# Optimization experiments

Hardware: AMD Instinct MI355X
Metric: run time of the kernel (lower is better)

## Reference

```python
import jax, jax.numpy as jnp
import numpy as np

LN_EPS = 1e-5
NORM_EPS = 1e-12  # F.normalize eps


def _l2norm(x):
    # torch F.normalize(p=2, dim=-1): x / max(||x||, eps)
    n = jnp.sqrt(jnp.sum(x * x, axis=-1, keepdims=True))
    return x / jnp.maximum(n, NORM_EPS)


def setup_inputs() -> dict:
    key = jax.random.key(0)
    D, R, H = 256, 32, 64  # d_model, rank, d_model//4
    B, C, P = 32, 64, 96
    ks = jax.random.split(key, 16)
    s = 0.05
    return {
        "x": jax.random.normal(ks[0], (B * C, P, D), jnp.float32),
        "ln_gamma": jnp.ones((D,), jnp.float32),
        "ln_beta": jnp.zeros((D,), jnp.float32),
        "Wd": jax.random.normal(ks[1], (D, R), jnp.float32) * s,
        "bd": jax.random.normal(ks[2], (R,), jnp.float32) * s,
        "Wq": jax.random.normal(ks[3], (R, R), jnp.float32) * s,
        "Wk": jax.random.normal(ks[4], (R, R), jnp.float32) * s,
        "Wv": jax.random.normal(ks[5], (R, R), jnp.float32) * s,
        "Wg": jax.random.normal(ks[6], (R, R), jnp.float32) * s,
        "bg": jax.random.normal(ks[7], (R,), jnp.float32) * s,
        "Wu": jax.random.normal(ks[8], (R, D), jnp.float32) * s,
        "bu": jax.random.normal(ks[9], (D,), jnp.float32) * s,
        "W1": jax.random.normal(ks[10], (D, H), jnp.float32) * s,
        "b1": jax.random.normal(ks[11], (H,), jnp.float32) * s,
        "W2": jax.random.normal(ks[12], (H, D), jnp.float32) * s,
        "b2": jnp.full((D,), -5.0, jnp.float32),  # gate_init bias
        "B": B,
        "C": C,
    }


def reference(x, ln_gamma, ln_beta, Wd, bd, Wq, Wk, Wv, Wg, bg, Wu, bu, W1, b1, W2, b2, B, C):
    BC, P, D = x.shape
    # [B*C, P, D] -> [B*P, C, D] channel-mixing layout
    h = x.reshape(B, C, P, D).transpose(0, 2, 1, 3).reshape(B * P, C, D)

    # LayerNorm over D (biased variance, as in torch LayerNorm)
    mu = jnp.mean(h, axis=-1, keepdims=True)
    var = jnp.var(h, axis=-1, keepdims=True)
    h_norm = (h - mu) * jax.lax.rsqrt(var + LN_EPS) * ln_gamma + ln_beta

    # bottleneck projection to rank R
    h_low = h_norm @ Wd + bd  # [BP, C, R]

    # Hydra linear attention: cosine-normalized Q/K, sum-pooled K*V global feature
    Q = _l2norm(h_low @ Wq)
    K = _l2norm(h_low @ Wk)
    V = h_low @ Wv
    global_feat = jnp.sum(K * V, axis=1, keepdims=True)  # [BP, 1, R]
    h_attn = Q * global_feat

    # content gate and up-projection
    gate_c = jax.nn.sigmoid(h_low @ Wg + bg)
    mixed = (h_attn * gate_c) @ Wu + bu  # [BP, C, D]

    # AdaptiveGate: unbiased variance over channel dim (torch .var default ddof=1)
    chan_var = jnp.var(h, axis=1, ddof=1)  # [BP, D]
    gate_logits = jax.nn.gelu(chan_var @ W1 + b1, approximate=False) @ W2 + b2
    gate = jax.nn.sigmoid(gate_logits)[:, None, :]  # [BP, 1, D]

    out = h + gate * mixed
    # back to [B*C, P, D]
    return out.reshape(B, P, C, D).transpose(0, 2, 1, 3).reshape(BC, P, D)
```

## Files before the change

kernel.cpp:

```cpp
#include <hip/hip_runtime.h>
#include <hip/hip_bf16.h>

#define DD 256
#define RR 32
#define CC 64
#define PB 96
#define NT 1024

typedef __attribute__((ext_vector_type(8))) short short8;
typedef __attribute__((ext_vector_type(4))) float f32x4;

__device__ __forceinline__ short f2bf(float f) {
    return __builtin_bit_cast(short, __float2bfloat16(f));
}
__device__ __forceinline__ float b2f(unsigned short s) {
    union { unsigned u; float f; } v; v.u = ((unsigned)s) << 16;
    return v.f;
}

__device__ __forceinline__ int hswz(int c, int d) {
    return c * 256 + (d ^ ((c & 7) << 3));
}
__device__ __forceinline__ int nswz(int r, int k) {
    return r * 32 + (k ^ (((r >> 1) & 3) << 3));
}

__global__ __launch_bounds__(1024, 1)
void prep_kernel(const float* __restrict__ ln_g, const float* __restrict__ ln_b,
                 const float* __restrict__ Wd, const float* __restrict__ bd,
                 const float* __restrict__ Wq, const float* __restrict__ Wk,
                 const float* __restrict__ Wv, const float* __restrict__ Wg,
                 const float* __restrict__ Wu,
                 const float* __restrict__ W1, const float* __restrict__ W2,
                 short* __restrict__ wsF1, short* __restrict__ wsF2,
                 short* __restrict__ wsF3, float* __restrict__ wsLN,
                 float* __restrict__ wsW1T, float* __restrict__ wsW2T)
{
    __shared__ float redp[2048];
    const int t = threadIdx.x;
    {
        const int r = t >> 5, dblk = t & 31;
        float sa = 0.f, sb = 0.f;
        #pragma unroll
        for (int j = 0; j < 8; ++j) {
            const int d = dblk * 8 + j;
            const float wd = Wd[d * RR + r];
            sa += ln_g[d] * wd;
            sb += ln_b[d] * wd;
        }
        redp[r * 32 + dblk]        = sa;
        redp[1024 + r * 32 + dblk] = sb;
    }
    {
        const int f = t >> 6, l = t & 63;
        const int rt = f >> 3, step = f & 7;
        const int r = rt * 16 + (l & 15);
        short8 v;
        #pragma unroll
        for (int j = 0; j < 8; ++j) {
            const int d = step * 32 + (l >> 4) * 8 + j;
            v[j] = f2bf(ln_g[d] * Wd[d * RR + r]);
        }
        *(short8*)&wsF1[f * 512 + l * 8] = v;
    }
    if (t < 512) {
        const int f = t >> 6, l = t & 63;
        const int m = f >> 1, half = f & 1;
        const float* Wm = (m == 0) ? Wq : (m == 1) ? Wk : (m == 2) ? Wv : Wg;
        const int rout = half * 16 + (l & 15);
        short8 v;
        #pragma unroll
        for (int j = 0; j < 8; ++j) {
            const int rin = (l >> 4) * 8 + j;
            v[j] = f2bf(Wm[rin * RR + rout]);
        }
        *(short8*)&wsF2[f * 512 + l * 8] = v;
    }
    {
        const int f = t >> 6, l = t & 63;
        const int d = f * 16 + (l & 15);
        short8 v;
        #pragma unroll
        for (int j = 0; j < 8; ++j) {
            const int r = (l >> 4) * 8 + j;
            v[j] = f2bf(Wu[r * DD + d]);
        }
        *(short8*)&wsF3[f * 512 + l * 8] = v;
    }
    #pragma unroll
    for (int rep = 0; rep < 16; ++rep) {
        const int id = rep * 1024 + t;
        const int j = id >> 8, d = id & 255;
        wsW1T[j * 256 + d] = W1[d * 64 + j];
    }
    #pragma unroll
    for (int rep = 0; rep < 16; ++rep) {
        const int id = rep * 1024 + t;
        const int d = id >> 6, j = id & 63;
        wsW2T[d * 64 + j] = W2[j * 256 + d];
    }
    __syncthreads();
    if (t < 32) {
        float s = 0.f;
        #pragma unroll
        for (int g = 0; g < 32; ++g) s += redp[t * 32 + g];
        wsLN[t] = s;
    } else if (t < 64) {
        const int r = t - 32;
        float s = 0.f;
        #pragma unroll
        for (int g = 0; g < 32; ++g) s += redp[1024 + r * 32 + g];
        wsLN[t] = s + bd[r];
    }
}

__global__ __launch_bounds__(NT, 8)
void hydra_kernel(const float* __restrict__ x,
                  const short* __restrict__ wsF1, const short* __restrict__ wsF2,
                  const short* __restrict__ wsF3, const float* __restrict__ wsLN,
                  const float* __restrict__ wsW1T, const float* __restrict__ wsW2T,
                  const float* __restrict__ bg,
                  const float* __restrict__ bu,
                  const float* __restrict__ b1, const float* __restrict__ b2,
                  float* __restrict__ out)
{
    __shared__ short hbf[CC * DD];
    __shared__ short qg[CC * RR];
    __shared__ short lowbuf[CC * RR];
    __shared__ float redA[1024];
    __shared__ float redB[2048];
    __shared__ float redC[1024];
    __shared__ float mu_s[CC], rstd_s[CC];
    __shared__ float cv_s[DD], gate_s[DD];
    __shared__ float hid_s[64];
    __shared__ float ln_a[RR], ln_bv[RR];

    const int t    = threadIdx.x;
    const int lane = t & 63;
    const int w    = t >> 6;
    const int bp   = blockIdx.x;
    const int b    = bp / PB;
    const int p    = bp - b * PB;
    const size_t rowbase = (size_t)(b * CC) * PB * DD + (size_t)p * DD;

    #pragma unroll
    for (int i = 0; i < 4; ++i) {
        const int c = w * 4 + i;
        const float4 v = *(const float4*)(x + rowbase + (size_t)c * (PB * DD) + 4 * lane);
        float s1 = v.x + v.y + v.z + v.w;
        float s2 = v.x * v.x + v.y * v.y + v.z * v.z + v.w * v.w;
        s1 += __shfl_xor(s1, 1, 64); s2 += __shfl_xor(s2, 1, 64);
        s1 += __shfl_xor(s1, 2, 64); s2 += __shfl_xor(s2, 2, 64);
        s1 += __shfl_xor(s1, 4, 64); s2 += __shfl_xor(s2, 4, 64);
        if ((lane & 7) == 0)
            *(float2*)&redC[(c * 8 + (lane >> 3)) * 2] = make_float2(s1, s2);
        ushort4 pk;
        pk.x = (unsigned short)f2bf(v.x); pk.y = (unsigned short)f2bf(v.y);
        pk.z = (unsigned short)f2bf(v.z); pk.w = (unsigned short)f2bf(v.w);
        *(ushort4*)&hbf[hswz(c, 4 * lane)] = pk;
    }
    if (t < 32)              ln_a[t]       = wsLN[t];
    else if (t < 64)         ln_bv[t - 32] = wsLN[t];
    __syncthreads();

    f32x4 s3acc = {0.f, 0.f, 0.f, 0.f};
    if (w < 8) {
        const int ct = w >> 1, rt = w & 1;
        const int arow = ct * 16 + (lane & 15);
        const int kofs = (lane >> 4) * 8;
        const short* fB = wsF1 + rt * 8 * 512 + lane * 8;
        #pragma unroll
        for (int step = 0; step < 8; ++step) {
            const short8 bf = *(const short8*)(fB + step * 512);
            const short8 a  = *(const short8*)&hbf[hswz(arow, step * 32 + kofs)];
            s3acc = __builtin_amdgcn_mfma_f32_16x16x32_bf16(a, bf, s3acc, 0, 0, 0);
        }
    } else {
        const int idx = t - 512;
        const int dp  = idx & 127;
        const int rg  = idx >> 7;
        const int d0  = dp * 2;
        float s1a = 0.f, s1b = 0.f, s2a = 0.f, s2b = 0.f;
        #pragma unroll
        for (int i = 0; i < 16; ++i) {
            const int c = rg * 16 + i;
            const ushort2 u = *(const ushort2*)&hbf[hswz(c, d0)];
            const float va = b2f(u.x), vb = b2f(u.y);
            s1a += va; s2a += va * va;
            s1b += vb; s2b += vb * vb;
        }
        *(float2*)&redB[rg * 256 + d0]        = make_float2(s1a, s1b);
        *(float2*)&redB[1024 + rg * 256 + d0] = make_float2(s2a, s2b);
        if (idx < 64) {
            const int c = idx;
            float s1 = 0.f, s2 = 0.f;
            #pragma unroll
            for (int g = 0; g < 8; ++g) {
                const float2 pr = *(const float2*)&redC[(c * 8 + g) * 2];
                s1 += pr.x; s2 += pr.y;
            }
            const float mu = s1 * (1.f / 256.f);
            mu_s[c]   = mu;
            rstd_s[c] = rsqrtf(s2 * (1.f / 256.f) - mu * mu + 1e-5f);
        }
    }
    __syncthreads();

    if (w < 8) {
        const int ct = w >> 1, rt = w & 1;
        const int col = rt * 16 + (lane & 15);
        const float la = ln_a[col], lb = ln_bv[col];
        #pragma unroll
        for (int i = 0; i < 4; ++i) {
            const int c = ct * 16 + (lane >> 4) * 4 + i;
            const float rs = rstd_s[c];
            const float hl = rs * s3acc[i] - rs * mu_s[c] * la + lb;
            lowbuf[nswz(c, col)] = f2bf(hl);
        }
    } else if (t < 768) {
        const int d = t - 512;
        const float S1 = redB[d] + redB[256 + d] + redB[512 + d] + redB[768 + d];
        const float S2 = redB[1024 + d] + redB[1280 + d] + redB[1536 + d] + redB[1792 + d];
        cv_s[d] = (S2 - S1 * S1 * (1.f / 64.f)) * (1.f / 63.f);
    }
    __syncthreads();

    if (w < 8) {
        const int ct = w >> 1, pair = w & 1;
        const int mA = pair ? 1 : 0;
        const int mB = pair ? 2 : 3;
        const int arow = ct * 16 + (lane & 15);
        const int kofs = (lane >> 4) * 8;
        const short8 a = *(const short8*)&lowbuf[nswz(arow, kofs)];
        const short8 bA0 = *(const short8*)(wsF2 + (mA * 2 + 0) * 512 + lane * 8);
        const short8 bA1 = *(const short8*)(wsF2 + (mA * 2 + 1) * 512 + lane * 8);
        const short8 bB0 = *(const short8*)(wsF2 + (mB * 2 + 0) * 512 + lane * 8);
        const short8 bB1 = *(const short8*)(wsF2 + (mB * 2 + 1) * 512 + lane * 8);
        f32x4 aA0 = {0,0,0,0}, aA1 = {0,0,0,0}, aB0 = {0,0,0,0}, aB1 = {0,0,0,0};
        aA0 = __builtin_amdgcn_mfma_f32_16x16x32_bf16(a, bA0, aA0, 0, 0, 0);
        aA1 = __builtin_amdgcn_mfma_f32_16x16x32_bf16(a, bA1, aA1, 0, 0, 0);
        aB0 = __builtin_amdgcn_mfma_f32_16x16x32_bf16(a, bB0, aB0, 0, 0, 0);
        aB1 = __builtin_amdgcn_mfma_f32_16x16x32_bf16(a, bB1, aB1, 0, 0, 0);
        float qs[4];
        #pragma unroll
        for (int i = 0; i < 4; ++i) {
            float ss = aA0[i] * aA0[i] + aA1[i] * aA1[i];
            ss += __shfl_xor(ss, 1, 64);
            ss += __shfl_xor(ss, 2, 64);
            ss += __shfl_xor(ss, 4, 64);
            ss += __shfl_xor(ss, 8, 64);
            qs[i] = 1.f / fmaxf(sqrtf(ss), 1e-12f);
        }
        const int col0 = (lane & 15), col1 = 16 + (lane & 15);
        if (pair == 0) {
            const float bgv0 = bg[col0], bgv1 = bg[col1];
            #pragma unroll
            for (int i = 0; i < 4; ++i) {
                const int c = ct * 16 + (lane >> 4) * 4 + i;
                const float g0 = 1.f / (1.f + __expf(-(aB0[i] + bgv0)));
                const float g1 = 1.f / (1.f + __expf(-(aB1[i] + bgv1)));
                qg[c * 32 + col0] = f2bf(aA0[i] * qs[i] * g0);
                qg[c * 32 + col1] = f2bf(aA1[i] * qs[i] * g1);
            }
        } else {
            #pragma unroll
            for (int i = 0; i < 4; ++i) {
                const int c = ct * 16 + (lane >> 4) * 4 + i;
                redB[c * 32 + col0] = aA0[i] * qs[i] * aB0[i];
                redB[c * 32 + col1] = aA1[i] * qs[i] * aB1[i];
            }
        }
    } else {
        const int idx = t - 512;
        const int j = idx & 63, dg = idx >> 6;
        const float* w1row = wsW1T + j * 256 + dg * 32;
        float s = 0.f;
        #pragma unroll
        for (int ii = 0; ii < 8; ++ii) {
            const float4 wv = *(const float4*)(w1row + ii * 4);
            const float4 cvv = *(const float4*)&cv_s[dg * 32 + ii * 4];
            s += cvv.x * wv.x + cvv.y * wv.y + cvv.z * wv.z + cvv.w * wv.w;
        }
        redA[dg * 64 + j] = s;
    }
    __syncthreads();

    if (t < 64) {
        float s = b1[t];
        #pragma unroll
        for (int g = 0; g < 8; ++g) s += redA[g * 64 + t];
        hid_s[t] = 0.5f * s * (1.f + erff(s * 0.70710678118654752f));
    }
    if (t >= 256 && t < 512) {
        const int idx = t - 256;
        const int r = idx & 31, g = idx >> 5;
        float s = 0.f;
        #pragma unroll
        for (int i = 0; i < 8; ++i)
            s += redB[(g * 8 + i) * 32 + r];
        redA[512 + g * 32 + r] = s;
    }
    __syncthreads();

    {
        const int d = t & 255, jg = t >> 8;
        const float* w2row = wsW2T + d * 64 + jg * 16;
        float s = 0.f;
        #pragma unroll
        for (int ii = 0; ii < 4; ++ii) {
            const float4 wv = *(const float4*)(w2row + ii * 4);
            const float4 hv = *(const float4*)&hid_s[jg * 16 + ii * 4];
            s += hv.x * wv.x + hv.y * wv.y + hv.z * wv.z + hv.w * wv.w;
        }
        redB[jg * 256 + d] = s;
    }
    if (t < 256) {
        const int r = t & 31, c0 = t >> 5, c1 = (t >> 5) + 32;
        float gf = 0.f;
        #pragma unroll
        for (int g = 0; g < 8; ++g) gf += redA[512 + g * 32 + r];
        lowbuf[nswz(c0, r)] = f2bf(b2f((unsigned short)qg[c0 * 32 + r]) * gf);
        lowbuf[nswz(c1, r)] = f2bf(b2f((unsigned short)qg[c1 * 32 + r]) * gf);
    }
    __syncthreads();

    {
        const int ct = w & 3, dg = w >> 2;
        const int arow = ct * 16 + (lane & 15);
        const int kofs = (lane >> 4) * 8;
        const short8 a = *(const short8*)&lowbuf[nswz(arow, kofs)];
        #pragma unroll
        for (int j = 0; j < 4; ++j) {
            const int dt = dg * 4 + j;
            const int col = dt * 16 + (lane & 15);
            const short8 bf = *(const short8*)(wsF3 + dt * 512 + lane * 8);
            f32x4 acc = {0.f, 0.f, 0.f, 0.f};
            acc = __builtin_amdgcn_mfma_f32_16x16x32_bf16(a, bf, acc, 0, 0, 0);
            #pragma unroll
            for (int i = 0; i < 4; ++i) {
                const int c = ct * 16 + (lane >> 4) * 4 + i;
                hbf[hswz(c, col)] = f2bf(acc[i]);
            }
        }
    }
    if (t < 256) {
        const float s = redB[t] + redB[256 + t] + redB[512 + t] + redB[768 + t] + b2[t];
        gate_s[t] = 1.f / (1.f + __expf(-s));
    }
    __syncthreads();

    #pragma unroll
    for (int i = 0; i < 4; ++i) {
        const int c = w * 4 + i;
        const size_t off = rowbase + (size_t)c * (PB * DD) + 4 * lane;
        const float4 xv = *(const float4*)(x + off);
        const ushort4 m = *(const ushort4*)&hbf[hswz(c, 4 * lane)];
        const float4 g4 = *(const float4*)&gate_s[4 * lane];
        const float4 bu4 = *(const float4*)(bu + 4 * lane);
        float4 o;
        o.x = xv.x + g4.x * (b2f(m.x) + bu4.x);
        o.y = xv.y + g4.y * (b2f(m.y) + bu4.y);
        o.z = xv.z + g4.z * (b2f(m.z) + bu4.z);
        o.w = xv.w + g4.w * (b2f(m.w) + bu4.w);
        *(float4*)(out + off) = o;
    }
}

extern "C" void kernel_launch(void* const* d_in, const int* in_sizes, int n_in,
                              void* d_out, int out_size, void* d_ws, size_t ws_size,
                              hipStream_t stream) {
    (void)in_sizes; (void)n_in; (void)out_size; (void)ws_size;
    const float* x    = (const float*)d_in[0];
    const float* ln_g = (const float*)d_in[1];
    const float* ln_b = (const float*)d_in[2];
    const float* Wd   = (const float*)d_in[3];
    const float* bd   = (const float*)d_in[4];
    const float* Wq   = (const float*)d_in[5];
    const float* Wk   = (const float*)d_in[6];
    const float* Wv   = (const float*)d_in[7];
    const float* Wg   = (const float*)d_in[8];
    const float* bg   = (const float*)d_in[9];
    const float* Wu   = (const float*)d_in[10];
    const float* bu   = (const float*)d_in[11];
    const float* W1   = (const float*)d_in[12];
    const float* b1   = (const float*)d_in[13];
    const float* W2   = (const float*)d_in[14];
    const float* b2   = (const float*)d_in[15];
    float* out = (float*)d_out;

    short* wsF1  = (short*)d_ws;
    short* wsF2  = wsF1 + 8192;
    short* wsF3  = wsF2 + 4096;
    float* wsLN  = (float*)(wsF1 + 20480);
    float* wsW1T = wsLN + 64;
    float* wsW2T = wsW1T + 16384;

    prep_kernel<<<dim3(1), dim3(1024), 0, stream>>>(
        ln_g, ln_b, Wd, bd, Wq, Wk, Wv, Wg, Wu, W1, W2,
        wsF1, wsF2, wsF3, wsLN, wsW1T, wsW2T);
    hydra_kernel<<<dim3(32 * PB), dim3(NT), 0, stream>>>(
        x, wsF1, wsF2, wsF3, wsLN, wsW1T, wsW2T, bg, bu, b1, b2, out);
}
```

Measured before the change: 171.4 us.

## Halve block size and restructure per-block work split and shared memory

Reduces the hydra kernel from 1024 to 512 threads per block, reassigning MFMA tiles so each of the first 4 waves computes the full 32-wide projections (Q/K/V/G all in one wave) while the other waves compute channel variance and the gate MLP directly from untransposed W1/W2. Shared buffers are aliased (qg/hlow reuse hbf, Abuf reuses pool_f) to cut LDS per block and allow more resident blocks. The prep kernel no longer transposes W1/W2. The aim is less LDS, fewer reduction stages and better occupancy, at the cost of more serial work per thread and strided global reads of W1.

```diff
diff --git a/kernel.cpp b/kernel.cpp
--- a/kernel.cpp
+++ b/kernel.cpp
@@ -5,7 +5,7 @@
 #define RR 32
 #define CC 64
 #define PB 96
-#define NT 1024
+#define NT 512
 
 typedef __attribute__((ext_vector_type(8))) short short8;
 typedef __attribute__((ext_vector_type(4))) float f32x4;
@@ -31,10 +31,8 @@
                  const float* __restrict__ Wq, const float* __restrict__ Wk,
                  const float* __restrict__ Wv, const float* __restrict__ Wg,
                  const float* __restrict__ Wu,
-                 const float* __restrict__ W1, const float* __restrict__ W2,
                  short* __restrict__ wsF1, short* __restrict__ wsF2,
-                 short* __restrict__ wsF3, float* __restrict__ wsLN,
-                 float* __restrict__ wsW1T, float* __restrict__ wsW2T)
+                 short* __restrict__ wsF3, float* __restrict__ wsLN)
 {
     __shared__ float redp[2048];
     const int t = threadIdx.x;
@@ -87,18 +85,6 @@
         }
         *(short8*)&wsF3[f * 512 + l * 8] = v;
     }
-    #pragma unroll
-    for (int rep = 0; rep < 16; ++rep) {
-        const int id = rep * 1024 + t;
-        const int j = id >> 8, d = id & 255;
-        wsW1T[j * 256 + d] = W1[d * 64 + j];
-    }
-    #pragma unroll
-    for (int rep = 0; rep < 16; ++rep) {
-        const int id = rep * 1024 + t;
-        const int d = id >> 6, j = id & 63;
-        wsW2T[d * 64 + j] = W2[j * 256 + d];
-    }
     __syncthreads();
     if (t < 32) {
         float s = 0.f;
@@ -114,26 +100,27 @@
     }
 }
 
-__global__ __launch_bounds__(NT, 8)
+__global__ __launch_bounds__(NT, 6)
 void hydra_kernel(const float* __restrict__ x,
                   const short* __restrict__ wsF1, const short* __restrict__ wsF2,
                   const short* __restrict__ wsF3, const float* __restrict__ wsLN,
-                  const float* __restrict__ wsW1T, const float* __restrict__ wsW2T,
-                  const float* __restrict__ bg,
-                  const float* __restrict__ bu,
-                  const float* __restrict__ b1, const float* __restrict__ b2,
+                  const float* __restrict__ bg, const float* __restrict__ bu,
+                  const float* __restrict__ W1, const float* __restrict__ b1,
+                  const float* __restrict__ W2, const float* __restrict__ b2,
                   float* __restrict__ out)
 {
     __shared__ short hbf[CC * DD];
-    __shared__ short qg[CC * RR];
-    __shared__ short lowbuf[CC * RR];
-    __shared__ float redA[1024];
-    __shared__ float redB[2048];
-    __shared__ float redC[1024];
+    __shared__ float pool_f[1024];
+    __shared__ float redA[128];
+    __shared__ float cv_s[DD];
+    __shared__ float gate_s[DD];
     __shared__ float mu_s[CC], rstd_s[CC];
-    __shared__ float cv_s[DD], gate_s[DD];
     __shared__ float hid_s[64];
     __shared__ float ln_a[RR], ln_bv[RR];
+
+    short* qg   = hbf;
+    short* hlow = hbf + 2048;
+    short* Abuf = (short*)pool_f;
 
     const int t    = threadIdx.x;
     const int lane = t & 63;
@@ -144,194 +131,172 @@
     const size_t rowbase = (size_t)(b * CC) * PB * DD + (size_t)p * DD;
 
     #pragma unroll
-    for (int i = 0; i < 4; ++i) {
-        const int c = w * 4 + i;
+    for (int i = 0; i < 8; ++i) {
+        const int c = w * 8 + i;
         const float4 v = *(const float4*)(x + rowbase + (size_t)c * (PB * DD) + 4 * lane);
         float s1 = v.x + v.y + v.z + v.w;
         float s2 = v.x * v.x + v.y * v.y + v.z * v.z + v.w * v.w;
         s1 += __shfl_xor(s1, 1, 64); s2 += __shfl_xor(s2, 1, 64);
         s1 += __shfl_xor(s1, 2, 64); s2 += __shfl_xor(s2, 2, 64);
         s1 += __shfl_xor(s1, 4, 64); s2 += __shfl_xor(s2, 4, 64);
-        if ((lane & 7) == 0)
-            *(float2*)&redC[(c * 8 + (lane >> 3)) * 2] = make_float2(s1, s2);
+        s1 += __shfl_xor(s1, 8, 64); s2 += __shfl_xor(s2, 8, 64);
+        if ((lane & 15) == 0)
+            *(float2*)&pool_f[(c * 4 + (lane >> 4)) * 2] = make_float2(s1, s2);
         ushort4 pk;
         pk.x = (unsigned short)f2bf(v.x); pk.y = (unsigned short)f2bf(v.y);
         pk.z = (unsigned short)f2bf(v.z); pk.w = (unsigned short)f2bf(v.w);
         *(ushort4*)&hbf[hswz(c, 4 * lane)] = pk;
     }
-    if (t < 32)              ln_a[t]       = wsLN[t];
-    else if (t < 64)         ln_bv[t - 32] = wsLN[t];
-    __syncthreads();
-
-    f32x4 s3acc = {0.f, 0.f, 0.f, 0.f};
-    if (w < 8) {
-        const int ct = w >> 1, rt = w & 1;
-        const int arow = ct * 16 + (lane & 15);
-        const int kofs = (lane >> 4) * 8;
-        const short* fB = wsF1 + rt * 8 * 512 + lane * 8;
-        #pragma unroll
-        for (int step = 0; step < 8; ++step) {
-            const short8 bf = *(const short8*)(fB + step * 512);
-            const short8 a  = *(const short8*)&hbf[hswz(arow, step * 32 + kofs)];
-            s3acc = __builtin_amdgcn_mfma_f32_16x16x32_bf16(a, bf, s3acc, 0, 0, 0);
-        }
-    } else {
-        const int idx = t - 512;
-        const int dp  = idx & 127;
-        const int rg  = idx >> 7;
-        const int d0  = dp * 2;
-        float s1a = 0.f, s1b = 0.f, s2a = 0.f, s2b = 0.f;
-        #pragma unroll
-        for (int i = 0; i < 16; ++i) {
-            const int c = rg * 16 + i;
-            const ushort2 u = *(const ushort2*)&hbf[hswz(c, d0)];
-            const float va = b2f(u.x), vb = b2f(u.y);
-            s1a += va; s2a += va * va;
-            s1b += vb; s2b += vb * vb;
-        }
-        *(float2*)&redB[rg * 256 + d0]        = make_float2(s1a, s1b);
-        *(float2*)&redB[1024 + rg * 256 + d0] = make_float2(s2a, s2b);
-        if (idx < 64) {
-            const int c = idx;
-            float s1 = 0.f, s2 = 0.f;
-            #pragma unroll
-            for (int g = 0; g < 8; ++g) {
-                const float2 pr = *(const float2*)&redC[(c * 8 + g) * 2];
-                s1 += pr.x; s2 += pr.y;
-            }
+    if (t < 32)            ln_a[t]       = wsLN[t];
+    else if (t < 64)       ln_bv[t - 32] = wsLN[t];
+    __syncthreads();
+
+    f32x4 acc0 = {0.f,0.f,0.f,0.f}, acc1 = {0.f,0.f,0.f,0.f};
+    if (w < 4) {
+        const int ct = w;
+        if (lane < 16) {
+            const int c = ct * 16 + lane;
+            const float2 p0 = *(const float2*)&pool_f[(c * 4 + 0) * 2];
+            const float2 p1 = *(const float2*)&pool_f[(c * 4 + 1) * 2];
+            const float2 p2 = *(const float2*)&pool_f[(c * 4 + 2) * 2];
+            const float2 p3 = *(const float2*)&pool_f[(c * 4 + 3) * 2];
+            const float s1 = p0.x + p1.x + p2.x + p3.x;
+            const float s2 = p0.y + p1.y + p2.y + p3.y;
             const float mu = s1 * (1.f / 256.f);
             mu_s[c]   = mu;
             rstd_s[c] = rsqrtf(s2 * (1.f / 256.f) - mu * mu + 1e-5f);
         }
-    }
-    __syncthreads();
-
-    if (w < 8) {
-        const int ct = w >> 1, rt = w & 1;
-        const int col = rt * 16 + (lane & 15);
-        const float la = ln_a[col], lb = ln_bv[col];
-        #pragma unroll
-        for (int i = 0; i < 4; ++i) {
-            const int c = ct * 16 + (lane >> 4) * 4 + i;
-            const float rs = rstd_s[c];
-            const float hl = rs * s3acc[i] - rs * mu_s[c] * la + lb;
-            lowbuf[nswz(c, col)] = f2bf(hl);
-        }
-    } else if (t < 768) {
-        const int d = t - 512;
-        const float S1 = redB[d] + redB[256 + d] + redB[512 + d] + redB[768 + d];
-        const float S2 = redB[1024 + d] + redB[1280 + d] + redB[1536 + d] + redB[1792 + d];
-        cv_s[d] = (S2 - S1 * S1 * (1.f / 64.f)) * (1.f / 63.f);
-    }
-    __syncthreads();
-
-    if (w < 8) {
-        const int ct = w >> 1, pair = w & 1;
-        const int mA = pair ? 1 : 0;
-        const int mB = pair ? 2 : 3;
         const int arow = ct * 16 + (lane & 15);
         const int kofs = (lane >> 4) * 8;
-        const short8 a = *(const short8*)&lowbuf[nswz(arow, kofs)];
-        const short8 bA0 = *(const short8*)(wsF2 + (mA * 2 + 0) * 512 + lane * 8);
-        const short8 bA1 = *(const short8*)(wsF2 + (mA * 2 + 1) * 512 + lane * 8);
-        const short8 bB0 = *(const short8*)(wsF2 + (mB * 2 + 0) * 512 + lane * 8);
-        const short8 bB1 = *(const short8*)(wsF2 + (mB * 2 + 1) * 512 + lane * 8);
-        f32x4 aA0 = {0,0,0,0}, aA1 = {0,0,0,0}, aB0 = {0,0,0,0}, aB1 = {0,0,0,0};
-        aA0 = __builtin_amdgcn_mfma_f32_16x16x32_bf16(a, bA0, aA0, 0, 0, 0);
-        aA1 = __builtin_amdgcn_mfma_f32_16x16x32_bf16(a, bA1, aA1, 0, 0, 0);
-        aB0 = __builtin_amdgcn_mfma_f32_16x16x32_bf16(a, bB0, aB0, 0, 0, 0);
-        aB1 = __builtin_amdgcn_mfma_f32_16x16x32_bf16(a, bB1, aB1, 0, 0, 0);
-        float qs[4];
-        #pragma unroll
-        for (int i = 0; i < 4; ++i) {
-            float ss = aA0[i] * aA0[i] + aA1[i] * aA1[i];
-            ss += __shfl_xor(ss, 1, 64);
-            ss += __shfl_xor(ss, 2, 64);
-            ss += __shfl_xor(ss, 4, 64);
-            ss += __shfl_xor(ss, 8, 64);
-            qs[i] = 1.f / fmaxf(sqrtf(ss), 1e-12f);
-        }
-        const int col0 = (lane & 15), col1 = 16 + (lane & 15);
-        if (pair == 0) {
-            const float bgv0 = bg[col0], bgv1 = bg[col1];
+        #pragma unroll
+        for (int step = 0; step < 8; ++step) {
+            const short8 a   = *(const short8*)&hbf[hswz(arow, step * 32 + kofs)];
+            const short8 bf0 = *(const short8*)(wsF1 + step * 512 + lane * 8);
+            const short8 bf1 = *(const short8*)(wsF1 + (8 + step) * 512 + lane * 8);
+            acc0 = __builtin_amdgcn_mfma_f32_16x16x32_bf16(a, bf0, acc0, 0, 0, 0);
+            acc1 = __builtin_amdgcn_mfma_f32_16x16x32_bf16(a, bf1, acc1, 0, 0, 0);
+        }
+    } else {
+        const int d = t - 256;
+        float s1 = 0.f, s2 = 0.f;
+        #pragma unroll 8
+        for (int c = 0; c < CC; ++c) {
+            const float v = b2f((unsigned short)hbf[hswz(c, d)]);
+            s1 += v; s2 += v * v;
+        }
+        cv_s[d] = (s2 - s1 * s1 * (1.f / 64.f)) * (1.f / 63.f);
+    }
+    __syncthreads();
+
+    if (w < 4) {
+        const int ct = w;
+        const int col0 = lane & 15, col1 = 16 + col0;
+        {
+            const float la0 = ln_a[col0], lb0 = ln_bv[col0];
+            const float la1 = ln_a[col1], lb1 = ln_bv[col1];
             #pragma unroll
             for (int i = 0; i < 4; ++i) {
                 const int c = ct * 16 + (lane >> 4) * 4 + i;
-                const float g0 = 1.f / (1.f + __expf(-(aB0[i] + bgv0)));
-                const float g1 = 1.f / (1.f + __expf(-(aB1[i] + bgv1)));
-                qg[c * 32 + col0] = f2bf(aA0[i] * qs[i] * g0);
-                qg[c * 32 + col1] = f2bf(aA1[i] * qs[i] * g1);
+                const float rs = rstd_s[c], mu = mu_s[c];
+                hlow[nswz(c, col0)] = f2bf(rs * acc0[i] - rs * mu * la0 + lb0);
+                hlow[nswz(c, col1)] = f2bf(rs * acc1[i] - rs * mu * la1 + lb1);
             }
-        } else {
-            #pragma unroll
-            for (int i = 0; i < 4; ++i) {
-                const int c = ct * 16 + (lane >> 4) * 4 + i;
-                redB[c * 32 + col0] = aA0[i] * qs[i] * aB0[i];
-                redB[c * 32 + col1] = aA1[i] * qs[i] * aB1[i];
-            }
+        }
+        const int arow = ct * 16 + col0;
+        const int kofs = (lane >> 4) * 8;
+        const short8 a = *(const short8*)&hlow[nswz(arow, kofs)];
+        const short8 bQ0 = *(const short8*)(wsF2 + 0 * 512 + lane * 8);
+        const short8 bQ1 = *(const short8*)(wsF2 + 1 * 512 + lane * 8);
+        const short8 bK0 = *(const short8*)(wsF2 + 2 * 512 + lane * 8);
+        const short8 bK1 = *(const short8*)(wsF2 + 3 * 512 + lane * 8);
+        const short8 bV0 = *(const short8*)(wsF2 + 4 * 512 + lane * 8);
+        const short8 bV1 = *(const short8*)(wsF2 + 5 * 512 + lane * 8);
+        const short8 bG0 = *(const short8*)(wsF2 + 6 * 512 + lane * 8);
+        const short8 bG1 = *(const short8*)(wsF2 + 7 * 512 + lane * 8);
+        f32x4 aQ0={0,0,0,0}, aQ1={0,0,0,0}, aK0={0,0,0,0}, aK1={0,0,0,0};
+        f32x4 aV0={0,0,0,0}, aV1={0,0,0,0}, aG0={0,0,0,0}, aG1={0,0,0,0};
+        aQ0 = __builtin_amdgcn_mfma_f32_16x16x32_bf16(a, bQ0, aQ0, 0, 0, 0);
+        aQ1 = __builtin_amdgcn_mfma_f32_16x16x32_bf16(a, bQ1, aQ1, 0, 0, 0);
+        aK0 = __builtin_amdgcn_mfma_f32_16x16x32_bf16(a, bK0, aK0, 0, 0, 0);
+        aK1 = __builtin_amdgcn_mfma_f32_16x16x32_bf16(a, bK1, aK1, 0, 0, 0);
+        aV0 = __builtin_amdgcn_mfma_f32_16x16x32_bf16(a, bV0, aV0, 0, 0, 0);
+        aV1 = __builtin_amdgcn_mfma_f32_16x16x32_bf16(a, bV1, aV1, 0, 0, 0);
+        aG0 = __builtin_amdgcn_mfma_f32_16x16x32_bf16(a, bG0, aG0, 0, 0, 0);
+        aG1 = __builtin_amdgcn_mfma_f32_16x16x32_bf16(a, bG1, aG1, 0, 0, 0);
+        float qs[4], ks[4];
+        #pragma unroll
+        for (int i = 0; i < 4; ++i) {
+            float sq = aQ0[i] * aQ0[i] + aQ1[i] * aQ1[i];
+            float sk = aK0[i] * aK0[i] + aK1[i] * aK1[i];
+            sq += __shfl_xor(sq, 1, 64); sk += __shfl_xor(sk, 1, 64);
+            sq += __shfl_xor(sq, 2, 64); sk += __shfl_xor(sk, 2, 64);
+            sq += __shfl_xor(sq, 4, 64); sk += __shfl_xor(sk, 4, 64);
+            sq += __shfl_xor(sq, 8, 64); sk += __shfl_xor(sk, 8, 64);
+            qs[i] = 1.f / fmaxf(sqrtf(sq), 1e-12f);
+            ks[i] = 1.f / fmaxf(sqrtf(sk), 1e-12f);
+        }
+        const float bgv0 = bg[col0], bgv1 = bg[col1];
+        float p0 = 0.f, p1 = 0.f;
+        #pragma unroll
+        for (int i = 0; i < 4; ++i) {
+            const int c = ct * 16 + (lane >> 4) * 4 + i;
+            const float g0 = 1.f / (1.f + __expf(-(aG0[i] + bgv0)));
+            const float g1 = 1.f / (1.f + __expf(-(aG1[i] + bgv1)));
+            qg[c * 32 + col0] = f2bf(aQ0[i] * qs[i] * g0);
+            qg[c * 32 + col1] = f2bf(aQ1[i] * qs[i] * g1);
+            p0 += (aK0[i] * ks[i]) * aV0[i];
+            p1 += (aK1[i] * ks[i]) * aV1[i];
+        }
+        p0 += __shfl_xor(p0, 16, 64); p1 += __shfl_xor(p1, 16, 64);
+        p0 += __shfl_xor(p0, 32, 64); p1 += __shfl_xor(p1, 32, 64);
+        if (lane < 16) {
+            redA[ct * 32 + lane]      = p0;
+            redA[ct * 32 + 16 + lane] = p1;
         }
     } else {
-        const int idx = t - 512;
-        const int j = idx & 63, dg = idx >> 6;
-        const float* w1row = wsW1T + j * 256 + dg * 32;
+        const int j = (w - 4) * 16 + (lane >> 2);
+        const int q = lane & 3;
         float s = 0.f;
-        #pragma unroll
-        for (int ii = 0; ii < 8; ++ii) {
-            const float4 wv = *(const float4*)(w1row + ii * 4);
-            const float4 cvv = *(const float4*)&cv_s[dg * 32 + ii * 4];
-            s += cvv.x * wv.x + cvv.y * wv.y + cvv.z * wv.z + cvv.w * wv.w;
-        }
-        redA[dg * 64 + j] = s;
-    }
-    __syncthreads();
-
-    if (t < 64) {
-        float s = b1[t];
-        #pragma unroll
-        for (int g = 0; g < 8; ++g) s += redA[g * 64 + t];
-        hid_s[t] = 0.5f * s * (1.f + erff(s * 0.70710678118654752f));
-    }
-    if (t >= 256 && t < 512) {
-        const int idx = t - 256;
-        const int r = idx & 31, g = idx >> 5;
-        float s = 0.f;
-        #pragma unroll
-        for (int i = 0; i < 8; ++i)
-            s += redB[(g * 8 + i) * 32 + r];
-        redA[512 + g * 32 + r] = s;
+        #pragma unroll 8
+        for (int i = 0; i < 64; ++i) {
+            const int d = q * 64 + i;
+            s += cv_s[d] * W1[d * 64 + j];
+        }
+        s += __shfl_xor(s, 1, 64);
+        s += __shfl_xor(s, 2, 64);
+        if (q == 0) {
+            const float z = s + b1[j];
+            hid_s[j] = 0.5f * z * (1.f + erff(z * 0.70710678118654752f));
+        }
+    }
+    __syncthreads();
+
+    if (t < 256) {
+        const int r = t & 31, cb = t >> 5;
+        const float gf = redA[r] + redA[32 + r] + redA[64 + r] + redA[96 + r];
+        #pragma unroll
+        for (int k = 0; k < 8; ++k) {
+            const int c = cb * 8 + k;
+            Abuf[nswz(c, r)] = f2bf(b2f((unsigned short)qg[c * 32 + r]) * gf);
+        }
+    } else {
+        const int d = t - 256;
+        float s = b2[d];
+        #pragma unroll 8
+        for (int j = 0; j < 64; ++j)
+            s += hid_s[j] * W2[j * DD + d];
+        gate_s[d] = 1.f / (1.f + __expf(-s));
     }
     __syncthreads();
 
     {
-        const int d = t & 255, jg = t >> 8;
-        const float* w2row = wsW2T + d * 64 + jg * 16;
-        float s = 0.f;
-        #pragma unroll
-        for (int ii = 0; ii < 4; ++ii) {
-            const float4 wv = *(const float4*)(w2row + ii * 4);
-            const float4 hv = *(const float4*)&hid_s[jg * 16 + ii * 4];
-            s += hv.x * wv.x + hv.y * wv.y + hv.z * wv.z + hv.w * wv.w;
-        }
-        redB[jg * 256 + d] = s;
-    }
-    if (t < 256) {
-        const int r = t & 31, c0 = t >> 5, c1 = (t >> 5) + 32;
-        float gf = 0.f;
-        #pragma unroll
-        for (int g = 0; g < 8; ++g) gf += redA[512 + g * 32 + r];
-        lowbuf[nswz(c0, r)] = f2bf(b2f((unsigned short)qg[c0 * 32 + r]) * gf);
-        lowbuf[nswz(c1, r)] = f2bf(b2f((unsigned short)qg[c1 * 32 + r]) * gf);
-    }
-    __syncthreads();
-
-    {
-        const int ct = w & 3, dg = w >> 2;
+        const int ct = w & 3, dgh = w >> 2;
         const int arow = ct * 16 + (lane & 15);
         const int kofs = (lane >> 4) * 8;
-        const short8 a = *(const short8*)&lowbuf[nswz(arow, kofs)];
-        #pragma unroll
-        for (int j = 0; j < 4; ++j) {
-            const int dt = dg * 4 + j;
+        const short8 a = *(const short8*)&Abuf[nswz(arow, kofs)];
+        #pragma unroll
+        for (int j = 0; j < 8; ++j) {
+            const int dt = dgh * 8 + j;
             const int col = dt * 16 + (lane & 15);
             const short8 bf = *(const short8*)(wsF3 + dt * 512 + lane * 8);
             f32x4 acc = {0.f, 0.f, 0.f, 0.f};
@@ -343,15 +308,11 @@
             }
         }
     }
-    if (t < 256) {
-        const float s = redB[t] + redB[256 + t] + redB[512 + t] + redB[768 + t] + b2[t];
-        gate_s[t] = 1.f / (1.f + __expf(-s));
-    }
     __syncthreads();
 
     #pragma unroll
-    for (int i = 0; i < 4; ++i) {
-        const int c = w * 4 + i;
+    for (int i = 0; i < 8; ++i) {
+        const int c = w * 8 + i;
         const size_t off = rowbase + (size_t)c * (PB * DD) + 4 * lane;
         const float4 xv = *(const float4*)(x + off);
         const ushort4 m = *(const ushort4*)&hbf[hswz(c, 4 * lane)];
@@ -388,16 +349,13 @@
     const float* b2   = (const float*)d_in[15];
     float* out = (float*)d_out;
 
-    short* wsF1  = (short*)d_ws;
-    short* wsF2  = wsF1 + 8192;
-    short* wsF3  = wsF2 + 4096;
-    float* wsLN  = (float*)(wsF1 + 20480);
-    float* wsW1T = wsLN + 64;
-    float* wsW2T = wsW1T + 16384;
+    short* wsF1 = (short*)d_ws;
+    short* wsF2 = wsF1 + 8192;
+    short* wsF3 = wsF2 + 4096;
+    float* wsLN = (float*)(wsF1 + 20480);
 
     prep_kernel<<<dim3(1), dim3(1024), 0, stream>>>(
-        ln_g, ln_b, Wd, bd, Wq, Wk, Wv, Wg, Wu, W1, W2,
-        wsF1, wsF2, wsF3, wsLN, wsW1T, wsW2T);
+        ln_g, ln_b, Wd, bd, Wq, Wk, Wv, Wg, Wu, wsF1, wsF2, wsF3, wsLN);
     hydra_kernel<<<dim3(32 * PB), dim3(NT), 0, stream>>>(
-        x, wsF1, wsF2, wsF3, wsLN, wsW1T, wsW2T, bg, bu, b1, b2, out);
-}
+        x, wsF1, wsF2, wsF3, wsLN, bg, bu, W1, b1, W2, b2, out);
+}
```

New measurement: 165.5 us. 1.04x faster.
